# Kernel optimization log

Measured on AMD Instinct MI355X. Metric: run time of the kernel, lower is better.

The kernel has to match this reference:

```python
import jax, jax.numpy as jnp
import numpy as np
import math

B, S, E, H = 2, 4096, 1024, 16
W = 256  # one-sided attention window (attention_window // 2)


def setup_inputs() -> dict:
    key = jax.random.key(0)
    ks = jax.random.split(key, 7)
    init = lambda k, shp: jax.random.normal(k, shp, jnp.float32) * 0.02
    return {
        "hidden_states": jax.random.normal(ks[0], (B, S, E), jnp.float32),
        "attention_mask": jnp.zeros((B, S), jnp.int32),  # 0 = local attention
        "q_w": init(ks[1], (E, E)), "q_b": jnp.zeros((E,), jnp.float32),
        "k_w": init(ks[2], (E, E)), "k_b": jnp.zeros((E,), jnp.float32),
        "v_w": init(ks[3], (E, E)), "v_b": jnp.zeros((E,), jnp.float32),
    }


def _banded_attention(hidden_states, attention_mask, q_w, q_b, k_w, k_b, v_w, v_b):
    D = E // H          # head dim
    w = W               # one-sided window
    nc = S // w         # number of query chunks of length w
    # Projections (torch Linear: x @ W.T + b); query pre-scaled by sqrt(head_dim)
    q = (hidden_states @ q_w.T + q_b) / math.sqrt(D)
    k = hidden_states @ k_w.T + k_b
    v = hidden_states @ v_w.T + v_b
    heads = lambda x: x.reshape(B, S, H, D).transpose(0, 2, 1, 3)  # [B,H,S,D]
    q, k, v = heads(q), heads(k), heads(v)

    qc = q.reshape(B, H, nc, w, D)                       # [B,H,nc,w,D]
    pad = lambda x: jnp.pad(x, ((0, 0), (0, 0), (w, w), (0, 0)))
    # chunk c of keys/values covers padded positions [c*w, c*w + 3w)
    idx = (jnp.arange(nc) * w)[:, None] + jnp.arange(3 * w)[None, :]  # [nc,3w]
    kc = pad(k)[:, :, idx]                               # [B,H,nc,3w,D]
    vc = pad(v)[:, :, idx]                               # [B,H,nc,3w,D]

    # banded scores: query x in chunk attends padded key y; rel offset = y-w-x
    scores = jnp.einsum('bhcxd,bhcyd->bhcxy', qc, kc)    # [B,H,nc,w,3w]

    # additive mask from attention_mask (!=0 -> -10000 at that key position)
    fm = jnp.where(attention_mask != 0, -10000.0, 0.0)   # [B,S]
    fmc = jnp.pad(fm, ((0, 0), (w, w)))[:, idx]          # [B,nc,3w]
    scores = scores + fmc[:, None, :, None, :]

    # validity: |rel| <= w (the 2w+1 band) and key index j in [0, S)
    x = jnp.arange(w)[:, None]                           # [w,1]
    y = jnp.arange(3 * w)[None, :]                       # [1,3w]
    rel = y - w - x                                      # [w,3w]
    j = (jnp.arange(nc) * w)[:, None, None] + (y - w)[None]  # [nc,1,3w] key idx
    valid = (jnp.abs(rel) <= w)[None] & (j >= 0) & (j < S)   # [nc,w,3w]
    scores = jnp.where(valid[None, None], scores, -jnp.inf)

    probs = jax.nn.softmax(scores.astype(jnp.float32), axis=-1)
    ctx = jnp.einsum('bhcxy,bhcyd->bhcxd', probs, vc)    # [B,H,nc,w,D]
    return ctx.reshape(B, H, S, D).transpose(0, 2, 1, 3).reshape(B, S, E)


def reference(hidden_states, attention_mask, q_w, q_b, k_w, k_b, v_w, v_b):
    return _banded_attention(hidden_states, attention_mask,
                             q_w, q_b, k_w, k_b, v_w, v_b)
```

## Files before the change

kernel.cpp:

```cpp
#include <hip/hip_runtime.h>
#include <math.h>

constexpr int Bn  = 2;
constexpr int Sn  = 4096;
constexpr int En  = 1024;
constexpr int Hn  = 16;
constexpr int Mtot = Bn * Sn;
constexpr int Kp  = 1024;
constexpr int PAD = 72;

typedef __bf16    bf16x8 __attribute__((ext_vector_type(8)));
typedef __bf16    bf16x4 __attribute__((ext_vector_type(4)));
typedef _Float16  f16x8  __attribute__((ext_vector_type(8)));
typedef _Float16  f16x4  __attribute__((ext_vector_type(4)));
typedef float     f32x4  __attribute__((ext_vector_type(4)));

__global__ void __launch_bounds__(256)
cvt_all_kernel(const float* __restrict__ hs,
               const float* __restrict__ qw, const float* __restrict__ kw,
               const float* __restrict__ vw,
               _Float16* __restrict__ hs16, _Float16* __restrict__ w16)
{
    const int bid = blockIdx.x;
    if (bid < 8192) {
        int t = bid * 256 + threadIdx.x;
        int m = t >> 8;
        int k = (t & 255) << 2;
        float4 x = *(const float4*)&hs[((size_t)m << 10) + k];
        f16x4 h;
        h[0] = (_Float16)x.x; h[1] = (_Float16)x.y;
        h[2] = (_Float16)x.z; h[3] = (_Float16)x.w;
        *(f16x4*)&hs16[((size_t)m << 10) + k] = h;
    } else {
        int t = (bid - 8192) * 256 + threadIdx.x;
        int gn = t >> 8;
        int k  = (t & 255) << 2;
        int p  = gn >> 10, n = gn & 1023;
        const float* src = (p == 0) ? qw : (p == 1) ? kw : vw;
        float4 x = *(const float4*)&src[((size_t)n << 10) + k];
        f16x4 h;
        h[0] = (_Float16)x.x; h[1] = (_Float16)x.y;
        h[2] = (_Float16)x.z; h[3] = (_Float16)x.w;
        *(f16x4*)&w16[((size_t)gn << 10) + k] = h;
    }
}

__device__ inline void load_lds16(const void* g, void* s) {
    __builtin_amdgcn_global_load_lds((const __attribute__((address_space(1))) void*)g,
                                     (__attribute__((address_space(3))) void*)s,
                                     16, 0, 0);
}

__device__ inline void block_sync() {
    asm volatile("" ::: "memory");
    __builtin_amdgcn_s_barrier();
    asm volatile("" ::: "memory");
}
__device__ inline void vm_wait8() { asm volatile("s_waitcnt vmcnt(8)" ::: "memory"); }
__device__ inline void vm_wait4() { asm volatile("s_waitcnt vmcnt(4)" ::: "memory"); }
__device__ inline void vm_wait0() { asm volatile("s_waitcnt vmcnt(0)" ::: "memory"); }

typedef _Float16 ldsAB_t[2][2][256][32];

template<int PM>
__device__ __forceinline__ void
qkv_body(ldsAB_t& As, ldsAB_t& Bs,
         const _Float16* __restrict__ A2, const _Float16* __restrict__ B2,
         const float* __restrict__ qb, const float* __restrict__ kb,
         const float* __restrict__ vb,
         __bf16* __restrict__ q16, __bf16* __restrict__ k16,
         __bf16* __restrict__ vt16, int n0)
{
    const int tid  = threadIdx.x;
    const int w    = tid >> 6;
    const int lane = tid & 63;
    const int wm   = w >> 2, wn = w & 3;
    const int mrow = lane & 15, quad = lane >> 4;
    const int m0   = blockIdx.x * 256;

    const int subrow = lane >> 2;
    const int gch    = ((lane & 3) ^ ((lane >> 3) & 3)) * 8;
    const _Float16* Ag = A2 + (size_t)(m0 + w * 32 + subrow) * Kp + gch;
    const _Float16* Bg = B2 + (size_t)(n0 + w * 32 + subrow) * Kp + gch;

    const int sl = (quad ^ ((mrow >> 1) & 3)) * 8;

    f32x4 acc[8][4] = {};

    auto stageA = [&](int kt, int bi, int kc) {
        const size_t goff = (size_t)kt * 64 + kc * 32;
#pragma unroll
        for (int l = 0; l < 2; l++)
            load_lds16(Ag + (size_t)l * 16 * Kp + goff, &As[bi][kc][w * 32 + l * 16][0]);
    };
    auto stageB = [&](int kt, int bi, int kc) {
        const size_t goff = (size_t)kt * 64 + kc * 32;
#pragma unroll
        for (int l = 0; l < 2; l++)
            load_lds16(Bg + (size_t)l * 16 * Kp + goff, &Bs[bi][kc][w * 32 + l * 16][0]);
    };
    auto ladder = [&](const f16x8* AF, const f16x8* BF, int r0) {
        __builtin_amdgcn_s_setprio(1);
#pragma unroll
        for (int ti = 0; ti < 4; ti++)
#pragma unroll
            for (int tj = 0; tj < 4; tj++) {
                if (PM == 0)
                    acc[r0 + ti][tj] = __builtin_amdgcn_mfma_f32_16x16x32_f16(
                        BF[tj], AF[ti], acc[r0 + ti][tj], 0, 0, 0);
                else
                    acc[r0 + ti][tj] = __builtin_amdgcn_mfma_f32_16x16x32_f16(
                        AF[ti], BF[tj], acc[r0 + ti][tj], 0, 0, 0);
            }
        __builtin_amdgcn_s_setprio(0);
    };

    constexpr int NT = Kp / 64;

    float4 bv4[4];
    const int p = n0 >> 10;
    {
        const float* bptr = (p == 0) ? qb : (p == 1) ? kb : vb;
#pragma unroll
        for (int tj = 0; tj < 4; tj++) {
            if (PM == 0) {
                const int fl = (n0 + wn * 64 + tj * 16 + quad * 4) & 1023;
                bv4[tj] = *(const float4*)&bptr[fl];
            } else {
                const int n = (n0 + wn * 64 + tj * 16 + mrow) & 1023;
                bv4[tj].x = bptr[n];
            }
        }
    }

    stageA(0, 0, 0); stageB(0, 0, 0);
    stageA(0, 0, 1); stageB(0, 0, 1);
    vm_wait4();
    block_sync();

    for (int kt = 0; kt < NT; ++kt) {
        const int rb = kt & 1, wb = rb ^ 1;
        const bool pre  = (kt + 1 < NT);
        const bool last = (kt + 1 == NT);
        f16x8 af[4], bf[4];

#pragma unroll
        for (int t = 0; t < 4; t++)
            af[t] = *(const f16x8*)&As[rb][0][wm * 128 + t * 16 + mrow][sl];
#pragma unroll
        for (int t = 0; t < 4; t++)
            bf[t] = *(const f16x8*)&Bs[rb][0][wn * 64 + t * 16 + mrow][sl];
        if (pre) { stageA(kt + 1, wb, 0); stageB(kt + 1, wb, 0); }
        block_sync();
        ladder(af, bf, 0);
        block_sync();

#pragma unroll
        for (int t = 0; t < 4; t++)
            af[t] = *(const f16x8*)&As[rb][0][wm * 128 + 64 + t * 16 + mrow][sl];
        if (pre) { stageA(kt + 1, wb, 1); stageB(kt + 1, wb, 1); }
        block_sync();
        ladder(af, bf, 4);
        if (last) vm_wait0(); else vm_wait8();
        block_sync();

#pragma unroll
        for (int t = 0; t < 4; t++)
            af[t] = *(const f16x8*)&As[rb][1][wm * 128 + t * 16 + mrow][sl];
#pragma unroll
        for (int t = 0; t < 4; t++)
            bf[t] = *(const f16x8*)&Bs[rb][1][wn * 64 + t * 16 + mrow][sl];
        block_sync();
        ladder(af, bf, 0);
        block_sync();

#pragma unroll
        for (int t = 0; t < 4; t++)
            af[t] = *(const f16x8*)&As[rb][1][wm * 128 + 64 + t * 16 + mrow][sl];
        block_sync();
        ladder(af, bf, 4);
        vm_wait4();
        block_sync();
    }

    if (PM == 0) {
        __bf16* dst = (p == 0) ? q16 : k16;
        const float scl = (p == 0) ? 0.125f : 1.0f;
#pragma unroll
        for (int ti = 0; ti < 8; ti++) {
            const int m  = m0 + wm * 128 + ti * 16 + mrow;
            const int bb = m >> 12, ss = m & 4095;
#pragma unroll
            for (int tj = 0; tj < 4; tj++) {
                const int fl = (n0 + wn * 64 + tj * 16 + quad * 4) & 1023;
                const int hh = fl >> 6, dd = fl & 63;
                bf16x4 o;
                o[0] = (__bf16)((acc[ti][tj][0] + bv4[tj].x) * scl);
                o[1] = (__bf16)((acc[ti][tj][1] + bv4[tj].y) * scl);
                o[2] = (__bf16)((acc[ti][tj][2] + bv4[tj].z) * scl);
                o[3] = (__bf16)((acc[ti][tj][3] + bv4[tj].w) * scl);
                *(bf16x4*)&dst[((size_t)(bb * Hn + hh) * Sn + ss) * 64 + dd] = o;
            }
        }
    } else {
#pragma unroll
        for (int tj = 0; tj < 4; tj++) {
            const int n  = n0 + wn * 64 + tj * 16 + mrow;
            const float bv = bv4[tj].x;
            const int hh = (n & 1023) >> 6, dd = n & 63;
#pragma unroll
            for (int ti = 0; ti < 8; ti++) {
                const int m  = m0 + wm * 128 + ti * 16 + quad * 4;
                const int bb = m >> 12, ss = m & 4095;
                bf16x4 pv4;
#pragma unroll
                for (int r = 0; r < 4; r++)
                    pv4[r] = (__bf16)(acc[ti][tj][r] + bv);
                *(bf16x4*)&vt16[((size_t)(bb * Hn + hh) * 64 + dd) * Sn + ss] = pv4;
            }
        }
    }
}

__global__ void __launch_bounds__(512, 2)
qkv_fused_kernel(const _Float16* __restrict__ A2, const _Float16* __restrict__ B2,
                 const float* __restrict__ qb, const float* __restrict__ kb,
                 const float* __restrict__ vb,
                 __bf16* __restrict__ q16, __bf16* __restrict__ k16,
                 __bf16* __restrict__ vt16)
{
    __shared__ ldsAB_t As, Bs;
    const int by = blockIdx.y;
    if (by < 8)
        qkv_body<0>(As, Bs, A2, B2, qb, kb, vb, q16, k16, vt16, by * 256);
    else
        qkv_body<1>(As, Bs, A2, B2, qb, kb, vb, q16, k16, vt16,
                    2048 + (by - 8) * 256);
}

__global__ void __launch_bounds__(256, 2)
banded_attn_kernel(const __bf16* __restrict__ q16, const __bf16* __restrict__ k16,
                   const __bf16* __restrict__ vt16, const int* __restrict__ mask,
                   float* __restrict__ out)
{
    __shared__ __bf16 Kt[2][64 * PAD];
    __shared__ __bf16 Vt[2][64 * PAD];
    __shared__ __bf16 Pt[4][64 * PAD];
    __shared__ float  Msh[768];

    const int c = blockIdx.x, h = blockIdx.y, b = blockIdx.z;
    const int bh = b * Hn + h;
    const int i0 = c * 256;
    const int jwin0 = i0 - 256;
    const int tid  = threadIdx.x;
    const int wv   = tid >> 6;
    const int lane = tid & 63;
    const int quad = lane >> 4, mrow = lane & 15;

#pragma unroll
    for (int rep = 0; rep < 3; rep++) {
        int idx = rep * 256 + tid;
        int jg  = jwin0 + idx;
        float mv = -10000.f;
        if (jg >= 0 && jg < Sn)
            mv = (mask[b * Sn + jg] != 0) ? -10000.f : 0.f;
        Msh[idx] = mv;
    }

    bf16x8 qf[4][2];
    const __bf16* qbase = q16 + (((size_t)bh * Sn + i0 + wv * 64) << 6);
#pragma unroll
    for (int tjq = 0; tjq < 4; tjq++)
#pragma unroll
        for (int kc = 0; kc < 2; kc++)
            qf[tjq][kc] = *(const bf16x8*)(qbase + (16 * tjq + mrow) * 64 + 32 * kc + 8 * quad);

    const int sr = lane >> 3;
    const int sc = lane & 7;
    bf16x8 kreg0, kreg1, vreg0, vreg1;
    auto gload = [&](int st) {
        const int j0 = jwin0 + st * 64;
        const int r0 = wv * 16 + sr;
        const int r1 = wv * 16 + 8 + sr;
        int jk0 = j0 + r0; jk0 = jk0 < 0 ? 0 : (jk0 > Sn - 1 ? Sn - 1 : jk0);
        int jk1 = j0 + r1; jk1 = jk1 < 0 ? 0 : (jk1 > Sn - 1 ? Sn - 1 : jk1);
        kreg0 = *(const bf16x8*)&k16[(((size_t)bh * Sn + jk0) << 6) + sc * 8];
        kreg1 = *(const bf16x8*)&k16[(((size_t)bh * Sn + jk1) << 6) + sc * 8];
        int jv = j0 + sc * 8; jv = jv < 0 ? 0 : (jv > Sn - 8 ? Sn - 8 : jv);
        vreg0 = *(const bf16x8*)&vt16[((size_t)bh * 64 + r0) * Sn + jv];
        vreg1 = *(const bf16x8*)&vt16[((size_t)bh * 64 + r1) * Sn + jv];
    };
    auto swrite = [&](int buf) {
        *(bf16x8*)&Kt[buf][(wv * 16 + sr) * PAD + sc * 8]     = kreg0;
        *(bf16x8*)&Kt[buf][(wv * 16 + 8 + sr) * PAD + sc * 8] = kreg1;
        *(bf16x8*)&Vt[buf][(wv * 16 + sr) * PAD + sc * 8]     = vreg0;
        *(bf16x8*)&Vt[buf][(wv * 16 + 8 + sr) * PAD + sc * 8] = vreg1;
    };

    f32x4 acc_o[4][4] = {};
    float lrun[4] = {0.f, 0.f, 0.f, 0.f};
    __bf16* Pw = &Pt[wv][0];

    gload(0);
    swrite(0);
    __syncthreads();

    for (int st = 0; st < 12; st++) {
        const int buf = st & 1;
        if (st + 1 < 12) gload(st + 1);

        if (st >= wv && st <= wv + 8) {
            const __bf16* KtB = &Kt[buf][0];
            const __bf16* VtB = &Vt[buf][0];
            const bool edge = (st == wv) || (st == wv + 8);
#pragma unroll
            for (int ti = 0; ti < 4; ti++) {
                bf16x8 ak0 = *(const bf16x8*)&KtB[(16 * ti + mrow) * PAD + quad * 8];
                bf16x8 ak1 = *(const bf16x8*)&KtB[(16 * ti + mrow) * PAD + 32 + quad * 8];
                const int y0 = 64 * st + 16 * ti + 4 * quad;
                const f32x4 ms4 = *(const f32x4*)&Msh[y0];
#pragma unroll
                for (int tjq = 0; tjq < 4; tjq++) {
                    f32x4 s = ms4;
                    s = __builtin_amdgcn_mfma_f32_16x16x32_bf16(ak0, qf[tjq][0], s, 0, 0, 0);
                    s = __builtin_amdgcn_mfma_f32_16x16x32_bf16(ak1, qf[tjq][1], s, 0, 0, 0);
                    bf16x4 pk;
                    float psum = 0.f;
                    if (edge) {
                        const int xq = 64 * wv + 16 * tjq + mrow;
#pragma unroll
                        for (int r = 0; r < 4; r++) {
                            bool ok = ((unsigned)(y0 + r - xq) <= 512u);
                            float pv = ok ? __expf(s[r]) : 0.f;
                            psum += pv;
                            pk[r] = (__bf16)pv;
                        }
                    } else {
#pragma unroll
                        for (int r = 0; r < 4; r++) {
                            float pv = __expf(s[r]);
                            psum += pv;
                            pk[r] = (__bf16)pv;
                        }
                    }
                    lrun[tjq] += psum;
                    *(bf16x4*)&Pw[(16 * tjq + mrow) * PAD + 16 * ti + 4 * quad] = pk;
                }
            }
#pragma unroll
            for (int kc2 = 0; kc2 < 2; kc2++) {
                bf16x8 av[4];
#pragma unroll
                for (int dt = 0; dt < 4; dt++)
                    av[dt] = *(const bf16x8*)&VtB[(16 * dt + mrow) * PAD + kc2 * 32 + quad * 8];
#pragma unroll
                for (int tjq = 0; tjq < 4; tjq++) {
                    bf16x8 pf = *(const bf16x8*)&Pw[(16 * tjq + mrow) * PAD + kc2 * 32 + quad * 8];
#pragma unroll
                    for (int dt = 0; dt < 4; dt++)
                        acc_o[dt][tjq] = __builtin_amdgcn_mfma_f32_16x16x32_bf16(
                            av[dt], pf, acc_o[dt][tjq], 0, 0, 0);
                }
            }
        }

        if (st + 1 < 12) {
            swrite((st + 1) & 1);
            __syncthreads();
        }
    }

    float inv[4];
#pragma unroll
    for (int tjq = 0; tjq < 4; tjq++) {
        float l = lrun[tjq];
        l += __shfl_xor(l, 16);
        l += __shfl_xor(l, 32);
        inv[tjq] = 1.0f / l;
    }
#pragma unroll
    for (int dt = 0; dt < 4; dt++)
#pragma unroll
        for (int tjq = 0; tjq < 4; tjq++) {
            f32x4 o = acc_o[dt][tjq];
            o[0] *= inv[tjq]; o[1] *= inv[tjq]; o[2] *= inv[tjq]; o[3] *= inv[tjq];
            float* dst = out + ((size_t)(b * Sn + i0 + wv * 64 + 16 * tjq + mrow)) * En
                             + h * 64 + 16 * dt + 4 * quad;
            *(f32x4*)dst = o;
        }
}

extern "C" void kernel_launch(void* const* d_in, const int* in_sizes, int n_in,
                              void* d_out, int out_size, void* d_ws, size_t ws_size,
                              hipStream_t stream) {
    const float* hs  = (const float*)d_in[0];
    const int*  mask = (const int*)d_in[1];
    const float* qw  = (const float*)d_in[2];
    const float* qb  = (const float*)d_in[3];
    const float* kw  = (const float*)d_in[4];
    const float* kb  = (const float*)d_in[5];
    const float* vw  = (const float*)d_in[6];
    const float* vb  = (const float*)d_in[7];
    float* out = (float*)d_out;

    _Float16* hs16 = (_Float16*)d_ws;
    _Float16* w16  = (_Float16*)((char*)d_ws + (size_t)16777216);
    __bf16*   q16  = (__bf16*)((char*)d_ws + (size_t)23068672);
    __bf16*   k16  = (__bf16*)((char*)d_ws + (size_t)39845888);
    __bf16*   vt16 = (__bf16*)((char*)d_ws + (size_t)56623104);

    cvt_all_kernel<<<8192 + 3072, 256, 0, stream>>>(hs, qw, kw, vw, hs16, w16);

    dim3 pgrid(Mtot / 256, 12);
    qkv_fused_kernel<<<pgrid, 512, 0, stream>>>(hs16, w16, qb, kb, vb,
                                                q16, k16, vt16);

    dim3 agrid(Sn / 256, Hn, Bn);
    banded_attn_kernel<<<agrid, 256, 0, stream>>>(q16, k16, vt16, mask, out);
}
```

Measured before the change: 220.8 us.

## Halve QKV GEMM LDS buffers and raise occupancy to four blocks per CU

The QKV projection GEMM drops its double-buffered LDS tiles (2x2x256x32 per operand) for a single buffer split into two K-halves. Loads of one half now overlap compute on the other, with fewer barriers per k-step. Launch bounds go from 2 to 4 blocks per CU, so more workgroups can hide latency through occupancy instead of intra-block prefetch. In exchange, each block has less prefetch depth, and the tighter register budget may cause spills with a 32-accumulator-tile MFMA body.

```diff
diff --git a/kernel.cpp b/kernel.cpp
--- a/kernel.cpp
+++ b/kernel.cpp
@@ -56,11 +56,10 @@
     __builtin_amdgcn_s_barrier();
     asm volatile("" ::: "memory");
 }
-__device__ inline void vm_wait8() { asm volatile("s_waitcnt vmcnt(8)" ::: "memory"); }
 __device__ inline void vm_wait4() { asm volatile("s_waitcnt vmcnt(4)" ::: "memory"); }
 __device__ inline void vm_wait0() { asm volatile("s_waitcnt vmcnt(0)" ::: "memory"); }
 
-typedef _Float16 ldsAB_t[2][2][256][32];
+typedef _Float16 ldsAB_t[2][256][32];
 
 template<int PM>
 __device__ __forceinline__ void
@@ -87,17 +86,14 @@
 
     f32x4 acc[8][4] = {};
 
-    auto stageA = [&](int kt, int bi, int kc) {
+    auto stage = [&](int kt, int kc) {
         const size_t goff = (size_t)kt * 64 + kc * 32;
 #pragma unroll
         for (int l = 0; l < 2; l++)
-            load_lds16(Ag + (size_t)l * 16 * Kp + goff, &As[bi][kc][w * 32 + l * 16][0]);
-    };
-    auto stageB = [&](int kt, int bi, int kc) {
-        const size_t goff = (size_t)kt * 64 + kc * 32;
+            load_lds16(Ag + (size_t)l * 16 * Kp + goff, &As[kc][w * 32 + l * 16][0]);
 #pragma unroll
         for (int l = 0; l < 2; l++)
-            load_lds16(Bg + (size_t)l * 16 * Kp + goff, &Bs[bi][kc][w * 32 + l * 16][0]);
+            load_lds16(Bg + (size_t)l * 16 * Kp + goff, &Bs[kc][w * 32 + l * 16][0]);
     };
     auto ladder = [&](const f16x8* AF, const f16x8* BF, int r0) {
         __builtin_amdgcn_s_setprio(1);
@@ -133,53 +129,41 @@
         }
     }
 
-    stageA(0, 0, 0); stageB(0, 0, 0);
-    stageA(0, 0, 1); stageB(0, 0, 1);
-    vm_wait4();
-    block_sync();
+    stage(0, 0);
 
     for (int kt = 0; kt < NT; ++kt) {
-        const int rb = kt & 1, wb = rb ^ 1;
-        const bool pre  = (kt + 1 < NT);
-        const bool last = (kt + 1 == NT);
         f16x8 af[4], bf[4];
 
-#pragma unroll
-        for (int t = 0; t < 4; t++)
-            af[t] = *(const f16x8*)&As[rb][0][wm * 128 + t * 16 + mrow][sl];
-#pragma unroll
-        for (int t = 0; t < 4; t++)
-            bf[t] = *(const f16x8*)&Bs[rb][0][wn * 64 + t * 16 + mrow][sl];
-        if (pre) { stageA(kt + 1, wb, 0); stageB(kt + 1, wb, 0); }
+        stage(kt, 1);
+        vm_wait4();
         block_sync();
+#pragma unroll
+        for (int t = 0; t < 4; t++)
+            af[t] = *(const f16x8*)&As[0][wm * 128 + t * 16 + mrow][sl];
+#pragma unroll
+        for (int t = 0; t < 4; t++)
+            bf[t] = *(const f16x8*)&Bs[0][wn * 64 + t * 16 + mrow][sl];
         ladder(af, bf, 0);
+#pragma unroll
+        for (int t = 0; t < 4; t++)
+            af[t] = *(const f16x8*)&As[0][wm * 128 + 64 + t * 16 + mrow][sl];
+        ladder(af, bf, 4);
         block_sync();
 
-#pragma unroll
-        for (int t = 0; t < 4; t++)
-            af[t] = *(const f16x8*)&As[rb][0][wm * 128 + 64 + t * 16 + mrow][sl];
-        if (pre) { stageA(kt + 1, wb, 1); stageB(kt + 1, wb, 1); }
+        if (kt + 1 < NT) { stage(kt + 1, 0); vm_wait4(); }
+        else             { vm_wait0(); }
         block_sync();
+#pragma unroll
+        for (int t = 0; t < 4; t++)
+            af[t] = *(const f16x8*)&As[1][wm * 128 + t * 16 + mrow][sl];
+#pragma unroll
+        for (int t = 0; t < 4; t++)
+            bf[t] = *(const f16x8*)&Bs[1][wn * 64 + t * 16 + mrow][sl];
+        ladder(af, bf, 0);
+#pragma unroll
+        for (int t = 0; t < 4; t++)
+            af[t] = *(const f16x8*)&As[1][wm * 128 + 64 + t * 16 + mrow][sl];
         ladder(af, bf, 4);
-        if (last) vm_wait0(); else vm_wait8();
-        block_sync();
-
-#pragma unroll
-        for (int t = 0; t < 4; t++)
-            af[t] = *(const f16x8*)&As[rb][1][wm * 128 + t * 16 + mrow][sl];
-#pragma unroll
-        for (int t = 0; t < 4; t++)
-            bf[t] = *(const f16x8*)&Bs[rb][1][wn * 64 + t * 16 + mrow][sl];
-        block_sync();
-        ladder(af, bf, 0);
-        block_sync();
-
-#pragma unroll
-        for (int t = 0; t < 4; t++)
-            af[t] = *(const f16x8*)&As[rb][1][wm * 128 + 64 + t * 16 + mrow][sl];
-        block_sync();
-        ladder(af, bf, 4);
-        vm_wait4();
         block_sync();
     }
 
@@ -222,7 +206,7 @@
     }
 }
 
-__global__ void __launch_bounds__(512, 2)
+__global__ void __launch_bounds__(512, 4)
 qkv_fused_kernel(const _Float16* __restrict__ A2, const _Float16* __restrict__ B2,
                  const float* __restrict__ qb, const float* __restrict__ kb,
                  const float* __restrict__ vb,
```

Result: slower. 610.8 us (+176.6%).
